# Kernel tuning notes

Measured on AMD Instinct MI355X. Metric: run time of the kernel, lower is better.

The kernel has to match this reference:

```python
import jax, jax.numpy as jnp
import numpy as np

B, L, HID, H, DH = 1, 2048, 1024, 16, 64
KW = 2  # d_conv
EPS = float(np.finfo(np.float32).eps)  # torch RMSNorm eps=None -> dtype eps


def _causal_dw_conv(x, w, b):
    # x: (B, L, D), w: (D, K), b: (D,). Depthwise causal conv, no activation.
    Bs, Ls, D = x.shape
    K = w.shape[1]
    xp = jnp.pad(x, ((0, 0), (K - 1, 0), (0, 0)))
    out = b
    for k in range(K):
        out = out + xp[:, k:k + Ls, :] * w[:, k]
    return out


def setup_inputs() -> dict:
    key = jax.random.key(0)
    ks = jax.random.split(key, 14)
    hidden_states = jax.random.normal(ks[0], (B, L, HID), jnp.float32)
    # masked_fill(attention_mask != 0, -inf): True above diagonal (future masked)
    attention_mask = jnp.triu(jnp.ones((L, L), dtype=bool), 1)[None, None]
    all_dim = 3 * H * DH  # q_size + 2*kv_size with KVH == H
    qkv_w = jax.random.normal(ks[1], (all_dim, HID), jnp.float32) * 0.02
    q_conv_w = jax.random.normal(ks[2], (H * DH, KW), jnp.float32) * 0.5
    q_conv_b = jax.random.normal(ks[3], (H * DH,), jnp.float32) * 0.02
    k_conv_w = jax.random.normal(ks[4], (H * DH, KW), jnp.float32) * 0.5
    k_conv_b = jax.random.normal(ks[5], (H * DH,), jnp.float32) * 0.02
    v_conv_w = jax.random.normal(ks[6], (H * DH, KW), jnp.float32) * 0.5
    v_conv_b = jax.random.normal(ks[7], (H * DH,), jnp.float32) * 0.02
    norm_w = jnp.ones((DH,), jnp.float32)
    A_log = jnp.log(jax.random.uniform(ks[8], (H,), jnp.float32, 1.0, 16.0))
    dt0 = jnp.exp(jax.random.uniform(ks[9], (H,), jnp.float32)
                  * (np.log(0.1) - np.log(0.001)) + np.log(0.001))
    dt0 = jnp.clip(dt0, 1e-4)
    dt_bias = dt0 + jnp.log(-jnp.expm1(-dt0))  # inverse softplus init
    dt_proj_w = jax.random.normal(ks[10], (H, HID), jnp.float32) * 0.02
    dt_proj_b = jnp.zeros((H,), jnp.float32)
    o_w = jax.random.normal(ks[11], (HID, H * DH), jnp.float32) * 0.02
    order_coeff = jnp.ones((1, H, 1, 1), jnp.float32)  # 1/cumprod(arange(1,2))
    return dict(hidden_states=hidden_states, attention_mask=attention_mask,
                qkv_w=qkv_w, q_conv_w=q_conv_w, q_conv_b=q_conv_b,
                k_conv_w=k_conv_w, k_conv_b=k_conv_b, v_conv_w=v_conv_w,
                v_conv_b=v_conv_b, norm_w=norm_w, A_log=A_log, dt_bias=dt_bias,
                dt_proj_w=dt_proj_w, dt_proj_b=dt_proj_b, o_w=o_w,
                order_coeff=order_coeff)


def reference(hidden_states, attention_mask, qkv_w, q_conv_w, q_conv_b,
              k_conv_w, k_conv_b, v_conv_w, v_conv_b, norm_w, A_log, dt_bias,
              dt_proj_w, dt_proj_b, o_w, order_coeff):
    qs = H * DH
    qkv = hidden_states @ qkv_w.T                    # (B, L, 3*H*DH)
    q = _causal_dw_conv(qkv[..., :qs], q_conv_w, q_conv_b)
    k = _causal_dw_conv(qkv[..., qs:2 * qs], k_conv_w, k_conv_b)
    v = _causal_dw_conv(qkv[..., 2 * qs:], v_conv_w, v_conv_b)
    # split heads -> (B, H, L, DH)
    q = q.reshape(B, L, H, DH).transpose(0, 2, 1, 3)
    k = k.reshape(B, L, H, DH).transpose(0, 2, 1, 3)
    v = v.reshape(B, L, H, DH).transpose(0, 2, 1, 3)
    # SSM-style gate: dt (B, L, H)
    dt = jax.nn.softplus(hidden_states @ dt_proj_w.T + dt_proj_b + dt_bias)
    v = v * jnp.swapaxes(dt, 1, 2)[..., None]        # value scaled by dt
    A = -jnp.exp(A_log)[None, None, :] * dt          # (B, L, H)
    A_cumsum = jnp.swapaxes(jnp.cumsum(A, axis=1), 1, 2)  # (B, H, L)
    diff = A_cumsum[:, :, :, None] - A_cumsum[:, :, None, :]  # (B, H, L, L)
    A_mask = jnp.exp(jnp.where(attention_mask, -jnp.inf, diff))
    # order == 1: Taylor series reduces to a single gated linear term
    scores = jnp.einsum('bhld,bhmd->bhlm', q, k) * A_mask * (1.0 / order_coeff)
    out = scores @ v                                  # (B, H, L, DH)
    # RMSNorm over head_dim
    out = out * jax.lax.rsqrt(jnp.mean(out * out, -1, keepdims=True) + EPS) * norm_w
    out = out.transpose(0, 2, 1, 3).reshape(B, L, H * DH)
    return out @ o_w.T
```

## Files before the change

kernel.cpp:

```cpp
#include <hip/hip_runtime.h>
#include <hip/hip_bf16.h>

#define L_SEQ 2048
#define HIDN  1024
#define NH    16
#define DHD   64
#define QKV_P 3200
#define QC_S  2048
#define LP    72

typedef float f4 __attribute__((ext_vector_type(4)));
typedef __bf16 bf16x8 __attribute__((ext_vector_type(8)));
typedef _Float16 half8 __attribute__((ext_vector_type(8)));

union H8 {
  half8 h;
  uint4 u4;
};

__device__ __forceinline__ float b2f(unsigned short u) {
  union { unsigned int i; float f; } c; c.i = ((unsigned int)u) << 16; return c.f;
}
__device__ __forceinline__ unsigned short f2b(float f) {
  union { float f; unsigned int i; } c; c.f = f;
  unsigned int r = c.i + 0x7FFFu + ((c.i >> 16) & 1u);
  return (unsigned short)(r >> 16);
}
__device__ __forceinline__ unsigned short f2h(float f) {
  union { _Float16 h; unsigned short u; } c; c.h = (_Float16)f; return c.u;
}

__global__ __launch_bounds__(256) void prep_kernel(
    const void* hs, const void* qkvw, const void* ow, const void* dtw,
    const void* qw, const void* qb, const void* kw, const void* kb,
    const void* vw, const void* vb, const void* nw, const void* al,
    const void* dtb, const void* dpb, const void* oc,
    unsigned short* __restrict__ hs_b, unsigned short* __restrict__ qkvw_b,
    unsigned short* __restrict__ ow_b,
    float* __restrict__ smallf, int* __restrict__ flag)
{
  __shared__ int cnt;
  if (threadIdx.x == 0) cnt = 0;
  __syncthreads();
  {
    const unsigned short* p = (const unsigned short*)hs;
    int c = 0;
    for (int i = threadIdx.x; i < 8192; i += 256)
      if (((p[i] >> 7) & 0xFFu) >= 140u) c++;
    atomicAdd(&cnt, c);
  }
  __syncthreads();
  const int f = (cnt >= 32) ? 1 : 0;
  if (blockIdx.x == 0 && threadIdx.x == 0) *flag = f;

  const int tid = blockIdx.x * 256 + threadIdx.x;
  const int nth = gridDim.x * 256;
  for (int i = tid; i < 1605632; i += nth) {
    const void* src; unsigned short* dst; int off;
    if (i < 524288)       { src = hs;   dst = hs_b;   off = i; }
    else if (i < 1310720) { src = qkvw; dst = qkvw_b; off = i - 524288; }
    else if (i < 1314816) { src = dtw;  dst = qkvw_b + 3072 * 1024; off = i - 1310720; }
    else if (i < 1343488) {
      *(ushort4*)(qkvw_b + 3088 * 1024 + (i - 1314816) * 4) = (ushort4){0, 0, 0, 0};
      continue;
    }
    else                  { src = ow;   dst = ow_b;   off = i - 1343488; }
    const int e = off * 4;
    if (f) {
      f4 v = *(const f4*)((const float*)src + e);
      ushort4 o;
      o.x = f2b(v[0]); o.y = f2b(v[1]); o.z = f2b(v[2]); o.w = f2b(v[3]);
      *(ushort4*)(dst + e) = o;
    } else {
      *(uint2*)(dst + e) = *(const uint2*)((const unsigned short*)src + e);
    }
  }
  const void* ptrs[11] = {qw, qb, kw, kb, vw, vb, nw, al, dtb, dpb, oc};
  const int sizes[11] = {2048, 1024, 2048, 1024, 2048, 1024, 64, 16, 16, 16, 16};
  int off = 0;
  for (int a = 0; a < 11; ++a) {
    for (int i = tid; i < sizes[a]; i += nth)
      smallf[off + i] = f ? ((const float*)ptrs[a])[i]
                          : b2f(((const unsigned short*)ptrs[a])[i]);
    off += sizes[a];
  }
}

__global__ __launch_bounds__(256) void gemm128(
    const unsigned short* __restrict__ A, const unsigned short* __restrict__ B,
    float* __restrict__ C, int M, int N, int K)
{
  __shared__ __align__(16) unsigned short As[128 * 40];
  __shared__ __align__(16) unsigned short Bs[128 * 40];
  const int t = threadIdx.x;
  const int w = t >> 6, lane = t & 63;
  const int quad = lane >> 4, l16 = lane & 15;
  const int wr = w >> 1, wc = w & 1;
  const int m0 = blockIdx.y * 128, n0 = blockIdx.x * 128;
  const int srow = t >> 1;
  const int scol = (t & 1) * 16;

  f4 acc[4][4];
#pragma unroll
  for (int i = 0; i < 4; ++i)
#pragma unroll
    for (int j = 0; j < 4; ++j) acc[i][j] = (f4){0.f, 0.f, 0.f, 0.f};

  const unsigned short* apg = A + (size_t)(m0 + srow) * K + scol;
  const unsigned short* bpg = B + (size_t)(n0 + srow) * K + scol;
  uint4 a0 = *(const uint4*)apg,       a1 = *(const uint4*)(apg + 8);
  uint4 b0 = *(const uint4*)bpg,       b1 = *(const uint4*)(bpg + 8);

  for (int k0 = 0; k0 < K; k0 += 32) {
    __syncthreads();
    *(uint4*)&As[srow * 40 + scol]     = a0;
    *(uint4*)&As[srow * 40 + scol + 8] = a1;
    *(uint4*)&Bs[srow * 40 + scol]     = b0;
    *(uint4*)&Bs[srow * 40 + scol + 8] = b1;
    __syncthreads();
    if (k0 + 32 < K) {
      a0 = *(const uint4*)(apg + k0 + 32); a1 = *(const uint4*)(apg + k0 + 40);
      b0 = *(const uint4*)(bpg + k0 + 32); b1 = *(const uint4*)(bpg + k0 + 40);
    }
    bf16x8 aF[4], bF[4];
#pragma unroll
    for (int i = 0; i < 4; ++i)
      aF[i] = *(const bf16x8*)&As[(wr * 64 + i * 16 + l16) * 40 + quad * 8];
#pragma unroll
    for (int j = 0; j < 4; ++j)
      bF[j] = *(const bf16x8*)&Bs[(wc * 64 + j * 16 + l16) * 40 + quad * 8];
#pragma unroll
    for (int i = 0; i < 4; ++i)
#pragma unroll
      for (int j = 0; j < 4; ++j)
        acc[i][j] = __builtin_amdgcn_mfma_f32_16x16x32_bf16(aF[i], bF[j], acc[i][j], 0, 0, 0);
  }

#pragma unroll
  for (int i = 0; i < 4; ++i)
#pragma unroll
    for (int j = 0; j < 4; ++j)
#pragma unroll
      for (int r = 0; r < 4; ++r) {
        int m = m0 + wr * 64 + i * 16 + quad * 4 + r;
        int n = n0 + wc * 64 + j * 16 + l16;
        C[(size_t)m * N + n] = acc[i][j][r];
      }
}

template <int MODE>
__global__ __launch_bounds__(256) void gemm_bt(
    const unsigned short* __restrict__ A, const unsigned short* __restrict__ B,
    void* __restrict__ Cv, int M, int N, int K, const int* __restrict__ flag)
{
  __shared__ __align__(16) short As[64 * 40];
  __shared__ __align__(16) short Bs[64 * 40];
  const int t = threadIdx.x;
  const int wave = t >> 6, lane = t & 63;
  const int quad = lane >> 4, l16 = lane & 15;
  const int m0 = blockIdx.y * 64, n0 = blockIdx.x * 64;
  const int srow = t >> 2, scol = (t & 3) * 8;
  f4 acc[4];
#pragma unroll
  for (int i = 0; i < 4; ++i) acc[i] = (f4){0.f, 0.f, 0.f, 0.f};
  const unsigned short* ap = A + (size_t)(m0 + srow) * K + scol;
  const unsigned short* bp = B + (size_t)(n0 + srow) * K + scol;
  for (int k0 = 0; k0 < K; k0 += 32) {
    uint4 av = *(const uint4*)(ap + k0);
    uint4 bv = *(const uint4*)(bp + k0);
    __syncthreads();
    *(uint4*)&As[srow * 40 + scol] = av;
    *(uint4*)&Bs[srow * 40 + scol] = bv;
    __syncthreads();
    bf16x8 af = *(const bf16x8*)&As[(wave * 16 + l16) * 40 + quad * 8];
#pragma unroll
    for (int nt = 0; nt < 4; ++nt) {
      bf16x8 bf = *(const bf16x8*)&Bs[(nt * 16 + l16) * 40 + quad * 8];
      acc[nt] = __builtin_amdgcn_mfma_f32_16x16x32_bf16(af, bf, acc[nt], 0, 0, 0);
    }
  }
  const int outf32 = (MODE == 0) ? 1 : (*flag ? 1 : 0);
#pragma unroll
  for (int nt = 0; nt < 4; ++nt) {
#pragma unroll
    for (int r = 0; r < 4; ++r) {
      int m = m0 + wave * 16 + quad * 4 + r;
      int n = n0 + nt * 16 + l16;
      if (outf32) ((float*)Cv)[(size_t)m * N + n] = acc[nt][r];
      else        ((unsigned short*)Cv)[(size_t)m * N + n] = f2b(acc[nt][r]);
    }
  }
}

__global__ __launch_bounds__(64) void cumsum_kernel(
    const float* __restrict__ qkvf, const float* __restrict__ smallf,
    float* __restrict__ dt_out, float* __restrict__ Ac)
{
  const int h = blockIdx.x;
  const int lane = threadIdx.x;
  const int base = lane * 32;
  const float dpb = smallf[9312 + h], dtb = smallf[9296 + h];
  const float nal = -expf(smallf[9280 + h]);
  float Av[32];
  float run = 0.f;
#pragma unroll
  for (int i = 0; i < 32; ++i) {
    const int l = base + i;
    float z = qkvf[(size_t)l * QKV_P + 3072 + h] + dpb + dtb;
    float dtv = (z > 20.f) ? z : log1pf(expf(z));
    dt_out[l * NH + h] = dtv;
    Av[i] = nal * dtv;
    run += Av[i];
  }
  float incl = run;
#pragma unroll
  for (int off = 1; off < 64; off <<= 1) {
    float n = __shfl_up(incl, off);
    if (lane >= off) incl += n;
  }
  float r2 = incl - run;
#pragma unroll
  for (int i = 0; i < 32; ++i) {
    r2 += Av[i];
    Ac[h * L_SEQ + base + i] = r2;
  }
}

__global__ __launch_bounds__(256) void conv_kernel(
    const float* __restrict__ qkvf, const float* __restrict__ smallf,
    const float* __restrict__ dt, unsigned short* __restrict__ qc,
    unsigned short* __restrict__ vt)
{
  if (blockIdx.x < 4096) {
    const int idx = blockIdx.x * 256 + threadIdx.x;
    const int l = idx >> 9;
    const int c = (idx & 511) * 4;
    f4 xc = *(const f4*)&qkvf[(size_t)l * QKV_P + c];
    f4 xp = (f4){0.f, 0.f, 0.f, 0.f};
    if (l > 0) xp = *(const f4*)&qkvf[(size_t)(l - 1) * QKV_P + c];
    const float* w; const float* b; int cb;
    if (c < HIDN) { w = smallf;        b = smallf + 2048; cb = c; }
    else          { w = smallf + 3072; b = smallf + 5120; cb = c - HIDN; }
    f4 o;
#pragma unroll
    for (int j = 0; j < 4; ++j)
      o[j] = b[cb + j] + xp[j] * w[(cb + j) * 2] + xc[j] * w[(cb + j) * 2 + 1];
    ushort4 st;
    st.x = f2h(o[0]); st.y = f2h(o[1]); st.z = f2h(o[2]); st.w = f2h(o[3]);
    *(ushort4*)&qc[(size_t)l * QC_S + c] = st;
  } else {
    __shared__ __align__(16) unsigned short Ts[64 * 68];
    const int bv = blockIdx.x - 4096;
    const int h = bv & 15;
    const int lt0 = bv >> 4;
    const int t = threadIdx.x;
    const int srow = t >> 2, cc = t & 3;
    const int l = lt0 * 64 + srow;
    const int cb = h * 64 + cc * 16;
    const float* w = smallf + 6144;
    const float* b = smallf + 8192;
    const float dtv = dt[l * NH + h];
    const float* xcp = &qkvf[(size_t)l * QKV_P + 2048 + cb];
    const float* xpp = &qkvf[(size_t)(l - 1) * QKV_P + 2048 + cb];
    unsigned short o16[16];
#pragma unroll
    for (int g = 0; g < 4; ++g) {
      f4 xc = *(const f4*)(xcp + g * 4);
      f4 xp = (f4){0.f, 0.f, 0.f, 0.f};
      if (l > 0) xp = *(const f4*)(xpp + g * 4);
#pragma unroll
      for (int j = 0; j < 4; ++j) {
        const int ch = cb + g * 4 + j;
        float o = b[ch] + xp[j] * w[ch * 2] + xc[j] * w[ch * 2 + 1];
        o16[g * 4 + j] = f2h(o * dtv);
      }
    }
    *(uint4*)&Ts[srow * 68 + cc * 16]     = *(const uint4*)&o16[0];
    *(uint4*)&Ts[srow * 68 + cc * 16 + 8] = *(const uint4*)&o16[8];
    __syncthreads();
    __align__(16) unsigned short o[16];
#pragma unroll
    for (int j = 0; j < 16; ++j) o[j] = Ts[(cc * 16 + j) * 68 + srow];
    unsigned short* op = vt + ((size_t)h * DHD + srow) * L_SEQ + lt0 * 64 + cc * 16;
    *(uint4*)op = *(const uint4*)&o[0];
    *(uint4*)(op + 8) = *(const uint4*)&o[8];
  }
}

__global__ __launch_bounds__(256) void attn_kernel(
    const unsigned short* __restrict__ qc,
    const unsigned short* __restrict__ vt,
    const float* __restrict__ Ac,
    const float* __restrict__ smallf,
    unsigned short* __restrict__ attn_out)
{
  const int n  = blockIdx.x + 32 * blockIdx.y;
  const int r_ = n & 7;
  const int q_ = n >> 3;
  const int h  = r_ + 8 * (q_ & 1);
  const int v_ = q_ >> 1;
  const int lt = (v_ < 16) ? v_ : (47 - v_);
  const int t  = threadIdx.x;
  const int w    = t >> 6;
  const int lane = t & 63;
  const int l16  = lane & 15;
  const int quad = lane >> 4;
  const int srow = t >> 2;
  const int cc   = t & 3;

  __shared__ __align__(16) unsigned short K_lds[2][64 * LP];
  __shared__ __align__(16) unsigned short V_lds[2][64 * LP];
  __shared__ __align__(16) unsigned short S_lds[64 * LP];

  const int l0 = lt * 64;
  const float rc = 1.0f / smallf[9328 + h];
  const float* Acp = Ac + h * L_SEQ;

  H8 qf0, qf1;
  {
    const unsigned short* qp =
        qc + (size_t)(l0 + w * 16 + l16) * QC_S + h * DHD + quad * 8;
    qf0.u4 = *(const uint4*)qp;
    qf1.u4 = *(const uint4*)(qp + 32);
  }
  float alv[4];
#pragma unroll
  for (int r = 0; r < 4; ++r) alv[r] = Acp[l0 + w * 16 + quad * 4 + r];

  f4 acc[4];
#pragma unroll
  for (int i = 0; i < 4; ++i) acc[i] = (f4){0.f, 0.f, 0.f, 0.f};

  const unsigned short* kgp =
      qc + (size_t)srow * QC_S + HIDN + h * DHD + cc * 16;
  const unsigned short* vgp =
      vt + ((size_t)h * DHD + srow) * L_SEQ + cc * 16;

  const int swo = srow * LP + cc * 16;

  uint4 k0v = *(const uint4*)kgp,       k1v = *(const uint4*)(kgp + 8);
  uint4 v0v = *(const uint4*)vgp,       v1v = *(const uint4*)(vgp + 8);
  float amv[4];
#pragma unroll
  for (int nt = 0; nt < 4; ++nt) amv[nt] = Acp[nt * 16 + l16];

  *(uint4*)&K_lds[0][swo]     = k0v;
  *(uint4*)&K_lds[0][swo + 8] = k1v;
  *(uint4*)&V_lds[0][swo]     = v0v;
  *(uint4*)&V_lds[0][swo + 8] = v1v;
  __syncthreads();

  int cur = 0;
  for (int it = 0; it <= lt; ++it) {
    uint4 nk0 = k0v, nk1 = k1v, nv0 = v0v, nv1 = v1v;
    float namv[4];
    const bool more = (it < lt);
    if (more) {
      const unsigned short* kp = kgp + (size_t)(it + 1) * 64 * QC_S;
      const unsigned short* vp = vgp + (size_t)(it + 1) * 64;
      nk0 = *(const uint4*)kp; nk1 = *(const uint4*)(kp + 8);
      nv0 = *(const uint4*)vp; nv1 = *(const uint4*)(vp + 8);
#pragma unroll
      for (int nt = 0; nt < 4; ++nt)
        namv[nt] = Acp[(it + 1) * 64 + nt * 16 + l16];
    }

    f4 s[4];
#pragma unroll
    for (int i = 0; i < 4; ++i) s[i] = (f4){0.f, 0.f, 0.f, 0.f};
#pragma unroll
    for (int ks = 0; ks < 2; ++ks) {
      H8 qk = ks ? qf1 : qf0;
#pragma unroll
      for (int nt = 0; nt < 4; ++nt) {
        H8 kf;
        kf.u4 = *(const uint4*)&K_lds[cur][(nt * 16 + l16) * LP + ks * 32 + quad * 8];
        s[nt] = __builtin_amdgcn_mfma_f32_16x16x32_f16(qk.h, kf.h, s[nt], 0, 0, 0);
      }
    }
    const int m0 = it * 64;
    if (it == lt) {
#pragma unroll
      for (int nt = 0; nt < 4; ++nt) {
        const int mg = m0 + nt * 16 + l16;
        const float am = amv[nt];
#pragma unroll
        for (int r = 0; r < 4; ++r) {
          const int lg = l0 + w * 16 + quad * 4 + r;
          float val = (mg <= lg) ? s[nt][r] * __expf(alv[r] - am) * rc : 0.0f;
          S_lds[(w * 16 + quad * 4 + r) * LP + nt * 16 + l16] = f2h(val);
        }
      }
    } else {
#pragma unroll
      for (int nt = 0; nt < 4; ++nt) {
        const float am = amv[nt];
#pragma unroll
        for (int r = 0; r < 4; ++r) {
          float val = s[nt][r] * __expf(alv[r] - am) * rc;
          S_lds[(w * 16 + quad * 4 + r) * LP + nt * 16 + l16] = f2h(val);
        }
      }
    }
#pragma unroll
    for (int ks = 0; ks < 2; ++ks) {
      H8 sa;
      sa.u4 = *(const uint4*)&S_lds[(w * 16 + l16) * LP + ks * 32 + quad * 8];
#pragma unroll
      for (int db = 0; db < 4; ++db) {
        H8 vb;
        vb.u4 = *(const uint4*)&V_lds[cur][(db * 16 + l16) * LP + ks * 32 + quad * 8];
        acc[db] = __builtin_amdgcn_mfma_f32_16x16x32_f16(sa.h, vb.h, acc[db], 0, 0, 0);
      }
    }
    if (more) {
      unsigned short* Kl = K_lds[cur ^ 1];
      unsigned short* Vl = V_lds[cur ^ 1];
      *(uint4*)&Kl[swo]     = nk0;
      *(uint4*)&Kl[swo + 8] = nk1;
      *(uint4*)&Vl[swo]     = nv0;
      *(uint4*)&Vl[swo + 8] = nv1;
#pragma unroll
      for (int nt = 0; nt < 4; ++nt) amv[nt] = namv[nt];
      __syncthreads();
      cur ^= 1;
    }
  }

#pragma unroll
  for (int r = 0; r < 4; ++r) {
    float p = acc[0][r] * acc[0][r] + acc[1][r] * acc[1][r]
            + acc[2][r] * acc[2][r] + acc[3][r] * acc[3][r];
#pragma unroll
    for (int off = 1; off < 16; off <<= 1) p += __shfl_xor(p, off);
    const float rn = rsqrtf(p * (1.0f / 64.0f) + 1.1920928955078125e-07f);
    unsigned short* op =
        attn_out + (size_t)(l0 + w * 16 + quad * 4 + r) * HIDN + h * DHD + l16;
#pragma unroll
    for (int ds = 0; ds < 4; ++ds)
      op[ds * 16] = f2b(acc[ds][r] * rn * smallf[9216 + ds * 16 + l16]);
  }
}

extern "C" void kernel_launch(void* const* d_in, const int* in_sizes, int n_in,
                              void* d_out, int out_size, void* d_ws, size_t ws_size,
                              hipStream_t stream)
{
  (void)in_sizes; (void)n_in; (void)out_size; (void)ws_size;
  const void* hs        = d_in[0];
  const void* qkv_w     = d_in[2];
  const void* q_conv_w  = d_in[3];
  const void* q_conv_b  = d_in[4];
  const void* k_conv_w  = d_in[5];
  const void* k_conv_b  = d_in[6];
  const void* v_conv_w  = d_in[7];
  const void* v_conv_b  = d_in[8];
  const void* norm_w    = d_in[9];
  const void* A_log     = d_in[10];
  const void* dt_bias   = d_in[11];
  const void* dt_proj_w = d_in[12];
  const void* dt_proj_b = d_in[13];
  const void* o_w       = d_in[14];
  const void* ordc      = d_in[15];

  char* ws = (char*)d_ws;
  int* flag             = (int*)ws;
  unsigned short* hs_b  = (unsigned short*)(ws + 256);
  unsigned short* qkvw_b= (unsigned short*)(ws + 4194560);
  unsigned short* ow_b  = (unsigned short*)(ws + 10748160);
  float* smallf         = (float*)(ws + 12845312);
  float* qkvf           = (float*)(ws + 12882688);
  unsigned short* qc_h  = (unsigned short*)(ws + 39097088);
  float* dtbuf          = (float*)(ws + 47485696);
  float* Acum           = (float*)(ws + 47616768);
  unsigned short* attnb = (unsigned short*)(ws + 47747840);
  unsigned short* vt_h  = (unsigned short*)(ws + 51942144);

  prep_kernel<<<1024, 256, 0, stream>>>(
      hs, qkv_w, o_w, dt_proj_w,
      q_conv_w, q_conv_b, k_conv_w, k_conv_b, v_conv_w, v_conv_b,
      norm_w, A_log, dt_bias, dt_proj_b, ordc,
      hs_b, qkvw_b, ow_b, smallf, flag);

  gemm128<<<dim3(QKV_P / 128, L_SEQ / 128), 256, 0, stream>>>(
      hs_b, qkvw_b, qkvf, L_SEQ, QKV_P, HIDN);
  cumsum_kernel<<<NH, 64, 0, stream>>>(qkvf, smallf, dtbuf, Acum);
  conv_kernel<<<4096 + 512, 256, 0, stream>>>(qkvf, smallf, dtbuf, qc_h, vt_h);
  attn_kernel<<<dim3(32, NH), 256, 0, stream>>>(qc_h, vt_h, Acum, smallf, attnb);
  gemm_bt<1><<<dim3(HIDN / 64, L_SEQ / 64), 256, 0, stream>>>(
      attnb, ow_b, d_out, L_SEQ, HIDN, HIDN, flag);
}
```

Measured before the change: 236.5 us.

## Split attention KV range across two blocks and fuse cumsum into conv

The attention kernel now launches twice as many blocks. Each handles half of the causal key-tile range for a query tile and writes unnormalized fp32 partial outputs. A new reduce kernel sums the two partials and applies the RMSNorm before the output GEMM, which is meant to balance load and raise occupancy on the long causal tiles. Separately, the dt/cumsum kernel is merged into the conv kernel as extra blocks, and the V path recomputes dt itself, removing a launch and the dt buffer at the cost of extra fp32 partial traffic and one more launch.

```diff
diff --git a/kernel.cpp b/kernel.cpp
--- a/kernel.cpp
+++ b/kernel.cpp
@@ -192,44 +192,10 @@
   }
 }
 
-__global__ __launch_bounds__(64) void cumsum_kernel(
-    const float* __restrict__ qkvf, const float* __restrict__ smallf,
-    float* __restrict__ dt_out, float* __restrict__ Ac)
-{
-  const int h = blockIdx.x;
-  const int lane = threadIdx.x;
-  const int base = lane * 32;
-  const float dpb = smallf[9312 + h], dtb = smallf[9296 + h];
-  const float nal = -expf(smallf[9280 + h]);
-  float Av[32];
-  float run = 0.f;
-#pragma unroll
-  for (int i = 0; i < 32; ++i) {
-    const int l = base + i;
-    float z = qkvf[(size_t)l * QKV_P + 3072 + h] + dpb + dtb;
-    float dtv = (z > 20.f) ? z : log1pf(expf(z));
-    dt_out[l * NH + h] = dtv;
-    Av[i] = nal * dtv;
-    run += Av[i];
-  }
-  float incl = run;
-#pragma unroll
-  for (int off = 1; off < 64; off <<= 1) {
-    float n = __shfl_up(incl, off);
-    if (lane >= off) incl += n;
-  }
-  float r2 = incl - run;
-#pragma unroll
-  for (int i = 0; i < 32; ++i) {
-    r2 += Av[i];
-    Ac[h * L_SEQ + base + i] = r2;
-  }
-}
-
 __global__ __launch_bounds__(256) void conv_kernel(
     const float* __restrict__ qkvf, const float* __restrict__ smallf,
-    const float* __restrict__ dt, unsigned short* __restrict__ qc,
-    unsigned short* __restrict__ vt)
+    unsigned short* __restrict__ qc, unsigned short* __restrict__ vt,
+    float* __restrict__ Ac)
 {
   if (blockIdx.x < 4096) {
     const int idx = blockIdx.x * 256 + threadIdx.x;
@@ -248,7 +214,7 @@
     ushort4 st;
     st.x = f2h(o[0]); st.y = f2h(o[1]); st.z = f2h(o[2]); st.w = f2h(o[3]);
     *(ushort4*)&qc[(size_t)l * QC_S + c] = st;
-  } else {
+  } else if (blockIdx.x < 4608) {
     __shared__ __align__(16) unsigned short Ts[64 * 68];
     const int bv = blockIdx.x - 4096;
     const int h = bv & 15;
@@ -259,7 +225,9 @@
     const int cb = h * 64 + cc * 16;
     const float* w = smallf + 6144;
     const float* b = smallf + 8192;
-    const float dtv = dt[l * NH + h];
+    const float z = qkvf[(size_t)l * QKV_P + 3072 + h]
+                  + smallf[9312 + h] + smallf[9296 + h];
+    const float dtv = (z > 20.f) ? z : log1pf(expf(z));
     const float* xcp = &qkvf[(size_t)l * QKV_P + 2048 + cb];
     const float* xpp = &qkvf[(size_t)(l - 1) * QKV_P + 2048 + cb];
     unsigned short o16[16];
@@ -284,6 +252,36 @@
     unsigned short* op = vt + ((size_t)h * DHD + srow) * L_SEQ + lt0 * 64 + cc * 16;
     *(uint4*)op = *(const uint4*)&o[0];
     *(uint4*)(op + 8) = *(const uint4*)&o[8];
+  } else {
+    const int h = blockIdx.x - 4608;
+    const int lane = threadIdx.x;
+    if (lane < 64) {
+      const int base = lane * 32;
+      const float dpb = smallf[9312 + h], dtb = smallf[9296 + h];
+      const float nal = -expf(smallf[9280 + h]);
+      float Av[32];
+      float run = 0.f;
+#pragma unroll
+      for (int i = 0; i < 32; ++i) {
+        const int l = base + i;
+        float z = qkvf[(size_t)l * QKV_P + 3072 + h] + dpb + dtb;
+        float dtv = (z > 20.f) ? z : log1pf(expf(z));
+        Av[i] = nal * dtv;
+        run += Av[i];
+      }
+      float incl = run;
+#pragma unroll
+      for (int off = 1; off < 64; off <<= 1) {
+        float n = __shfl_up(incl, off);
+        if (lane >= off) incl += n;
+      }
+      float r2 = incl - run;
+#pragma unroll
+      for (int i = 0; i < 32; ++i) {
+        r2 += Av[i];
+        Ac[h * L_SEQ + base + i] = r2;
+      }
+    }
   }
 }
 
@@ -292,14 +290,19 @@
     const unsigned short* __restrict__ vt,
     const float* __restrict__ Ac,
     const float* __restrict__ smallf,
-    unsigned short* __restrict__ attn_out)
-{
-  const int n  = blockIdx.x + 32 * blockIdx.y;
+    float* __restrict__ po)
+{
+  const int n  = blockIdx.x;
   const int r_ = n & 7;
-  const int q_ = n >> 3;
-  const int h  = r_ + 8 * (q_ & 1);
-  const int v_ = q_ >> 1;
-  const int lt = (v_ < 16) ? v_ : (47 - v_);
+  const int hh = (n >> 3) & 1;
+  const int k_ = n >> 4;
+  const int h  = r_ + 8 * hh;
+  const int lt = 31 - (k_ >> 1);
+  const int s_ = k_ & 1;
+  const int nT = lt + 1;
+  const int mS = s_ ? ((nT + 1) >> 1) : 0;
+  const int mE = s_ ? nT : ((nT + 1) >> 1);
+
   const int t  = threadIdx.x;
   const int w    = t >> 6;
   const int lane = t & 63;
@@ -335,111 +338,134 @@
       qc + (size_t)srow * QC_S + HIDN + h * DHD + cc * 16;
   const unsigned short* vgp =
       vt + ((size_t)h * DHD + srow) * L_SEQ + cc * 16;
-
   const int swo = srow * LP + cc * 16;
 
-  uint4 k0v = *(const uint4*)kgp,       k1v = *(const uint4*)(kgp + 8);
-  uint4 v0v = *(const uint4*)vgp,       v1v = *(const uint4*)(vgp + 8);
-  float amv[4];
-#pragma unroll
-  for (int nt = 0; nt < 4; ++nt) amv[nt] = Acp[nt * 16 + l16];
-
-  *(uint4*)&K_lds[0][swo]     = k0v;
-  *(uint4*)&K_lds[0][swo + 8] = k1v;
-  *(uint4*)&V_lds[0][swo]     = v0v;
-  *(uint4*)&V_lds[0][swo + 8] = v1v;
-  __syncthreads();
-
-  int cur = 0;
-  for (int it = 0; it <= lt; ++it) {
-    uint4 nk0 = k0v, nk1 = k1v, nv0 = v0v, nv1 = v1v;
-    float namv[4];
-    const bool more = (it < lt);
-    if (more) {
-      const unsigned short* kp = kgp + (size_t)(it + 1) * 64 * QC_S;
-      const unsigned short* vp = vgp + (size_t)(it + 1) * 64;
-      nk0 = *(const uint4*)kp; nk1 = *(const uint4*)(kp + 8);
-      nv0 = *(const uint4*)vp; nv1 = *(const uint4*)(vp + 8);
-#pragma unroll
-      for (int nt = 0; nt < 4; ++nt)
-        namv[nt] = Acp[(it + 1) * 64 + nt * 16 + l16];
-    }
-
-    f4 s[4];
-#pragma unroll
-    for (int i = 0; i < 4; ++i) s[i] = (f4){0.f, 0.f, 0.f, 0.f};
-#pragma unroll
-    for (int ks = 0; ks < 2; ++ks) {
-      H8 qk = ks ? qf1 : qf0;
-#pragma unroll
-      for (int nt = 0; nt < 4; ++nt) {
-        H8 kf;
-        kf.u4 = *(const uint4*)&K_lds[cur][(nt * 16 + l16) * LP + ks * 32 + quad * 8];
-        s[nt] = __builtin_amdgcn_mfma_f32_16x16x32_f16(qk.h, kf.h, s[nt], 0, 0, 0);
-      }
-    }
-    const int m0 = it * 64;
-    if (it == lt) {
-#pragma unroll
-      for (int nt = 0; nt < 4; ++nt) {
-        const int mg = m0 + nt * 16 + l16;
-        const float am = amv[nt];
-#pragma unroll
-        for (int r = 0; r < 4; ++r) {
-          const int lg = l0 + w * 16 + quad * 4 + r;
-          float val = (mg <= lg) ? s[nt][r] * __expf(alv[r] - am) * rc : 0.0f;
-          S_lds[(w * 16 + quad * 4 + r) * LP + nt * 16 + l16] = f2h(val);
+  if (mS < mE) {
+    uint4 k0v = *(const uint4*)(kgp + (size_t)mS * 64 * QC_S);
+    uint4 k1v = *(const uint4*)(kgp + (size_t)mS * 64 * QC_S + 8);
+    uint4 v0v = *(const uint4*)(vgp + (size_t)mS * 64);
+    uint4 v1v = *(const uint4*)(vgp + (size_t)mS * 64 + 8);
+    float amv[4];
+#pragma unroll
+    for (int nt = 0; nt < 4; ++nt) amv[nt] = Acp[mS * 64 + nt * 16 + l16];
+
+    *(uint4*)&K_lds[0][swo]     = k0v;
+    *(uint4*)&K_lds[0][swo + 8] = k1v;
+    *(uint4*)&V_lds[0][swo]     = v0v;
+    *(uint4*)&V_lds[0][swo + 8] = v1v;
+    __syncthreads();
+
+    int cur = 0;
+    for (int it = mS; it < mE; ++it) {
+      uint4 nk0 = k0v, nk1 = k1v, nv0 = v0v, nv1 = v1v;
+      float namv[4];
+      const bool more = (it + 1 < mE);
+      if (more) {
+        const unsigned short* kp = kgp + (size_t)(it + 1) * 64 * QC_S;
+        const unsigned short* vp = vgp + (size_t)(it + 1) * 64;
+        nk0 = *(const uint4*)kp; nk1 = *(const uint4*)(kp + 8);
+        nv0 = *(const uint4*)vp; nv1 = *(const uint4*)(vp + 8);
+#pragma unroll
+        for (int nt = 0; nt < 4; ++nt)
+          namv[nt] = Acp[(it + 1) * 64 + nt * 16 + l16];
+      }
+
+      f4 s[4];
+#pragma unroll
+      for (int i = 0; i < 4; ++i) s[i] = (f4){0.f, 0.f, 0.f, 0.f};
+#pragma unroll
+      for (int ks = 0; ks < 2; ++ks) {
+        H8 qk = ks ? qf1 : qf0;
+#pragma unroll
+        for (int nt = 0; nt < 4; ++nt) {
+          H8 kf;
+          kf.u4 = *(const uint4*)&K_lds[cur][(nt * 16 + l16) * LP + ks * 32 + quad * 8];
+          s[nt] = __builtin_amdgcn_mfma_f32_16x16x32_f16(qk.h, kf.h, s[nt], 0, 0, 0);
         }
       }
-    } else {
-#pragma unroll
-      for (int nt = 0; nt < 4; ++nt) {
-        const float am = amv[nt];
-#pragma unroll
-        for (int r = 0; r < 4; ++r) {
-          float val = s[nt][r] * __expf(alv[r] - am) * rc;
-          S_lds[(w * 16 + quad * 4 + r) * LP + nt * 16 + l16] = f2h(val);
+      const int m0 = it * 64;
+      if (it == lt) {
+#pragma unroll
+        for (int nt = 0; nt < 4; ++nt) {
+          const int mg = m0 + nt * 16 + l16;
+          const float am = amv[nt];
+#pragma unroll
+          for (int r = 0; r < 4; ++r) {
+            const int lg = l0 + w * 16 + quad * 4 + r;
+            float val = (mg <= lg) ? s[nt][r] * __expf(alv[r] - am) * rc : 0.0f;
+            S_lds[(w * 16 + quad * 4 + r) * LP + nt * 16 + l16] = f2h(val);
+          }
         }
-      }
-    }
-#pragma unroll
-    for (int ks = 0; ks < 2; ++ks) {
-      H8 sa;
-      sa.u4 = *(const uint4*)&S_lds[(w * 16 + l16) * LP + ks * 32 + quad * 8];
-#pragma unroll
-      for (int db = 0; db < 4; ++db) {
-        H8 vb;
-        vb.u4 = *(const uint4*)&V_lds[cur][(db * 16 + l16) * LP + ks * 32 + quad * 8];
-        acc[db] = __builtin_amdgcn_mfma_f32_16x16x32_f16(sa.h, vb.h, acc[db], 0, 0, 0);
-      }
-    }
-    if (more) {
-      unsigned short* Kl = K_lds[cur ^ 1];
-      unsigned short* Vl = V_lds[cur ^ 1];
-      *(uint4*)&Kl[swo]     = nk0;
-      *(uint4*)&Kl[swo + 8] = nk1;
-      *(uint4*)&Vl[swo]     = nv0;
-      *(uint4*)&Vl[swo + 8] = nv1;
-#pragma unroll
-      for (int nt = 0; nt < 4; ++nt) amv[nt] = namv[nt];
-      __syncthreads();
-      cur ^= 1;
-    }
-  }
-
+      } else {
+#pragma unroll
+        for (int nt = 0; nt < 4; ++nt) {
+          const float am = amv[nt];
+#pragma unroll
+          for (int r = 0; r < 4; ++r) {
+            float val = s[nt][r] * __expf(alv[r] - am) * rc;
+            S_lds[(w * 16 + quad * 4 + r) * LP + nt * 16 + l16] = f2h(val);
+          }
+        }
+      }
+#pragma unroll
+      for (int ks = 0; ks < 2; ++ks) {
+        H8 sa;
+        sa.u4 = *(const uint4*)&S_lds[(w * 16 + l16) * LP + ks * 32 + quad * 8];
+#pragma unroll
+        for (int db = 0; db < 4; ++db) {
+          H8 vb;
+          vb.u4 = *(const uint4*)&V_lds[cur][(db * 16 + l16) * LP + ks * 32 + quad * 8];
+          acc[db] = __builtin_amdgcn_mfma_f32_16x16x32_f16(sa.h, vb.h, acc[db], 0, 0, 0);
+        }
+      }
+      if (more) {
+        unsigned short* Kl = K_lds[cur ^ 1];
+        unsigned short* Vl = V_lds[cur ^ 1];
+        *(uint4*)&Kl[swo]     = nk0;
+        *(uint4*)&Kl[swo + 8] = nk1;
+        *(uint4*)&Vl[swo]     = nv0;
+        *(uint4*)&Vl[swo + 8] = nv1;
+#pragma unroll
+        for (int nt = 0; nt < 4; ++nt) amv[nt] = namv[nt];
+        __syncthreads();
+        cur ^= 1;
+      }
+    }
+  }
+
+  float* pout = po + (size_t)s_ * (L_SEQ * HIDN);
 #pragma unroll
   for (int r = 0; r < 4; ++r) {
-    float p = acc[0][r] * acc[0][r] + acc[1][r] * acc[1][r]
-            + acc[2][r] * acc[2][r] + acc[3][r] * acc[3][r];
-#pragma unroll
-    for (int off = 1; off < 16; off <<= 1) p += __shfl_xor(p, off);
-    const float rn = rsqrtf(p * (1.0f / 64.0f) + 1.1920928955078125e-07f);
-    unsigned short* op =
-        attn_out + (size_t)(l0 + w * 16 + quad * 4 + r) * HIDN + h * DHD + l16;
-#pragma unroll
-    for (int ds = 0; ds < 4; ++ds)
-      op[ds * 16] = f2b(acc[ds][r] * rn * smallf[9216 + ds * 16 + l16]);
-  }
+    float* op = pout + (size_t)(l0 + w * 16 + quad * 4 + r) * HIDN + h * DHD + l16;
+#pragma unroll
+    for (int db = 0; db < 4; ++db)
+      op[db * 16] = acc[db][r];
+  }
+}
+
+__global__ __launch_bounds__(256) void reduce_kernel(
+    const float* __restrict__ po, const float* __restrict__ smallf,
+    unsigned short* __restrict__ attn_out)
+{
+  const int l = blockIdx.x;
+  const int t = threadIdx.x;
+  const int col = t * 4;
+  const float* p0 = po + (size_t)l * HIDN + col;
+  const float* p1 = p0 + (size_t)L_SEQ * HIDN;
+  f4 a = *(const f4*)p0;
+  f4 b = *(const f4*)p1;
+  f4 o = a + b;
+  float p = o[0] * o[0] + o[1] * o[1] + o[2] * o[2] + o[3] * o[3];
+#pragma unroll
+  for (int off = 1; off < 16; off <<= 1) p += __shfl_xor(p, off);
+  const float rn = rsqrtf(p * (1.0f / 64.0f) + 1.1920928955078125e-07f);
+  const int d0 = col & 63;
+  ushort4 st;
+  st.x = f2b(o[0] * rn * smallf[9216 + d0]);
+  st.y = f2b(o[1] * rn * smallf[9216 + d0 + 1]);
+  st.z = f2b(o[2] * rn * smallf[9216 + d0 + 2]);
+  st.w = f2b(o[3] * rn * smallf[9216 + d0 + 3]);
+  *(ushort4*)&attn_out[(size_t)l * HIDN + col] = st;
 }
 
 extern "C" void kernel_launch(void* const* d_in, const int* in_sizes, int n_in,
@@ -471,10 +497,10 @@
   float* smallf         = (float*)(ws + 12845312);
   float* qkvf           = (float*)(ws + 12882688);
   unsigned short* qc_h  = (unsigned short*)(ws + 39097088);
-  float* dtbuf          = (float*)(ws + 47485696);
   float* Acum           = (float*)(ws + 47616768);
   unsigned short* attnb = (unsigned short*)(ws + 47747840);
   unsigned short* vt_h  = (unsigned short*)(ws + 51942144);
+  float* po             = (float*)(ws + 56136448);
 
   prep_kernel<<<1024, 256, 0, stream>>>(
       hs, qkv_w, o_w, dt_proj_w,
@@ -484,9 +510,9 @@
 
   gemm128<<<dim3(QKV_P / 128, L_SEQ / 128), 256, 0, stream>>>(
       hs_b, qkvw_b, qkvf, L_SEQ, QKV_P, HIDN);
-  cumsum_kernel<<<NH, 64, 0, stream>>>(qkvf, smallf, dtbuf, Acum);
-  conv_kernel<<<4096 + 512, 256, 0, stream>>>(qkvf, smallf, dtbuf, qc_h, vt_h);
-  attn_kernel<<<dim3(32, NH), 256, 0, stream>>>(qc_h, vt_h, Acum, smallf, attnb);
+  conv_kernel<<<4096 + 512 + 16, 256, 0, stream>>>(qkvf, smallf, qc_h, vt_h, Acum);
+  attn_kernel<<<1024, 256, 0, stream>>>(qc_h, vt_h, Acum, smallf, po);
+  reduce_kernel<<<L_SEQ, 256, 0, stream>>>(po, smallf, attnb);
   gemm_bt<1><<<dim3(HIDN / 64, L_SEQ / 64), 256, 0, stream>>>(
       attnb, ow_b, d_out, L_SEQ, HIDN, HIDN, flag);
 }
```

Measured after the change: 220.7 us, median of 2. -6.7%, faster.
